# Optimization experiments

Hardware: AMD Instinct MI355X
Metric: run time of the kernel (lower is better)

The kernel has to match this reference:

```python
import jax, jax.numpy as jnp
import numpy as np

NUM_HEADS = 16


def setup_inputs() -> dict:
    key = jax.random.key(0)
    k1, k2, k3 = jax.random.split(key, 3)
    B, L, H = 2, 2048, 1024
    return {
        "key": jax.random.normal(k1, (B, L, H), dtype=jnp.float32),
        "W_ctx": jax.random.normal(k2, (H, H), dtype=jnp.float32) * (1.0 / np.sqrt(H)),
        "b_ctx": jax.random.normal(k3, (H,), dtype=jnp.float32) * 0.01,
    }


def reference(key, W_ctx, b_ctx):
    # Note: the torch module defines q/k/v Linear layers but never calls them
    # in forward(); it reshapes the raw input into heads directly.
    B, L, H = key.shape
    dh = H // NUM_HEADS
    # [B, L, H] -> [B, nh, L, dh]
    x = key.reshape(B, L, NUM_HEADS, dh).transpose(0, 2, 1, 3)
    # QK^T then scale by sqrt(head_dim) (key.shape[-1] after head split)
    scores = jnp.einsum("bhqd,bhkd->bhqk", x, x) * (1.0 / np.float32(np.sqrt(dh)))
    attn = jax.nn.softmax(scores, axis=-1)  # dropout p treated as eval/identity
    ctx = jnp.einsum("bhqk,bhkd->bhqd", attn, x)
    # [B, nh, L, dh] -> [B, L, H]
    ctx = ctx.transpose(0, 2, 1, 3).reshape(B, L, H)
    # context_transform: nn.Linear(H, H, bias=True)
    return ctx @ W_ctx.T + b_ctx
```

## Files before the change

kernel.cpp:

```cpp
#include <hip/hip_runtime.h>
#include <stdint.h>

#define NH     16
#define LSEQ   2048
#define DH     64
#define HDIM   1024
#define BATCH  2

typedef __attribute__((ext_vector_type(8))) short bf16x8;
typedef __attribute__((ext_vector_type(4))) short bf16x4;
typedef __attribute__((ext_vector_type(8))) unsigned short u16x8;
typedef __attribute__((ext_vector_type(4))) float f32x4;

static __device__ inline unsigned short f2bs(float f) {
    union { float f; uint32_t u; } v; v.f = f;
    uint32_t u = v.u;
    return (unsigned short)((u + 0x7FFFu + ((u >> 16) & 1u)) >> 16);
}
static __device__ inline float bf2f(unsigned short s) {
    return __uint_as_float(((uint32_t)s) << 16);
}

#define GLOAD_LDS(gp, lp) \
    __builtin_amdgcn_global_load_lds((const __attribute__((address_space(1))) void*)(gp), \
                                     (__attribute__((address_space(3))) void*)(lp), 16, 0, 0)

#define QK_SCALE 0.42466083f

__global__ __launch_bounds__(256) void cvt_kernel(const float* __restrict__ W,
                                                  unsigned short* __restrict__ Wb,
                                                  int n) {
    int i = (blockIdx.x * 256 + threadIdx.x) * 4;
    if (i < n) {
        float4 f = *(const float4*)(W + i);
        *(ushort4*)(Wb + i) = make_ushort4(f2bs(f.x), f2bs(f.y), f2bs(f.z), f2bs(f.w));
    }
}

__global__ __launch_bounds__(256) void xcvt_kernel(const float* __restrict__ x,
                                                   unsigned short* __restrict__ xb,
                                                   unsigned short* __restrict__ xt) {
    const int lt = blockIdx.x, bh = blockIdx.y;
    const int b = bh >> 4, h = bh & 15;
    const int t = threadIdx.x;
    const int r = t >> 2, cp = t & 3;

    __shared__ __align__(16) unsigned short Sm[64][72];

    const float* src = x + ((size_t)(b * LSEQ + lt * 64 + r)) * HDIM + h * DH + cp * 16;
    float4 f0 = *(const float4*)(src);
    float4 f1 = *(const float4*)(src + 4);
    float4 f2 = *(const float4*)(src + 8);
    float4 f3 = *(const float4*)(src + 12);
    u16x8 lo, hi;
    lo[0]=f2bs(f0.x); lo[1]=f2bs(f0.y); lo[2]=f2bs(f0.z); lo[3]=f2bs(f0.w);
    lo[4]=f2bs(f1.x); lo[5]=f2bs(f1.y); lo[6]=f2bs(f1.z); lo[7]=f2bs(f1.w);
    hi[0]=f2bs(f2.x); hi[1]=f2bs(f2.y); hi[2]=f2bs(f2.z); hi[3]=f2bs(f2.w);
    hi[4]=f2bs(f3.x); hi[5]=f2bs(f3.y); hi[6]=f2bs(f3.z); hi[7]=f2bs(f3.w);
    u16x8 slo, shi;
    slo[0]=f2bs(f0.x*QK_SCALE); slo[1]=f2bs(f0.y*QK_SCALE); slo[2]=f2bs(f0.z*QK_SCALE); slo[3]=f2bs(f0.w*QK_SCALE);
    slo[4]=f2bs(f1.x*QK_SCALE); slo[5]=f2bs(f1.y*QK_SCALE); slo[6]=f2bs(f1.z*QK_SCALE); slo[7]=f2bs(f1.w*QK_SCALE);
    shi[0]=f2bs(f2.x*QK_SCALE); shi[1]=f2bs(f2.y*QK_SCALE); shi[2]=f2bs(f2.z*QK_SCALE); shi[3]=f2bs(f2.w*QK_SCALE);
    shi[4]=f2bs(f3.x*QK_SCALE); shi[5]=f2bs(f3.y*QK_SCALE); shi[6]=f2bs(f3.z*QK_SCALE); shi[7]=f2bs(f3.w*QK_SCALE);

    {
        unsigned short* kt = xb + ((size_t)(bh * 32 + lt)) * 4096;
        const int s  = r >> 4, la = r & 15;
        const int ks = cp >> 1, q0 = (cp & 1) * 2;
        *(u16x8*)(kt + ((s * 2 + ks) * 64 + q0 * 16 + la) * 8)       = slo;
        *(u16x8*)(kt + ((s * 2 + ks) * 64 + (q0 + 1) * 16 + la) * 8) = shi;
    }
    *(u16x8*)&Sm[r][cp * 16]     = lo;
    *(u16x8*)&Sm[r][cp * 16 + 8] = hi;
    __syncthreads();

    {
        const int dt = t >> 6, lane = t & 63;
        const int la = lane & 15, quad = lane >> 4;
        u16x8 g0, g1;
        #pragma unroll
        for (int kvt = 0; kvt < 2; ++kvt)
            #pragma unroll
            for (int j = 0; j < 4; ++j)
                g0[kvt * 4 + j] = Sm[kvt * 16 + quad * 4 + j][dt * 16 + la];
        #pragma unroll
        for (int kvt = 0; kvt < 2; ++kvt)
            #pragma unroll
            for (int j = 0; j < 4; ++j)
                g1[kvt * 4 + j] = Sm[(kvt + 2) * 16 + quad * 4 + j][dt * 16 + la];
        unsigned short* vt = xt + ((size_t)(bh * 32 + lt)) * 4096;
        *(u16x8*)(vt + (dt * 64 + lane) * 16)     = g0;
        *(u16x8*)(vt + (dt * 64 + lane) * 16 + 8) = g1;
    }
}

__global__ __launch_bounds__(256) void attn_kernel(const unsigned short* __restrict__ xb,
                                                   const unsigned short* __restrict__ xt,
                                                   unsigned short* __restrict__ po,
                                                   float* __restrict__ pl) {
    const int bh = blockIdx.x;
    const int qt = blockIdx.y;
    const int ks = blockIdx.z;
    const int tid = threadIdx.x;
    const int w = tid >> 6, lane = tid & 63;
    const int la = lane & 15, quad = lane >> 4;

    __shared__ __align__(16) unsigned short KL[2][4096];
    __shared__ __align__(16) unsigned short VL[2][4096];

    const unsigned short* xbh = xb + (size_t)bh * 32 * 4096;
    const unsigned short* xth = xt + (size_t)bh * 32 * 4096;
    const int qbase = qt * 128 + w * 32;
    const int t0 = ks * 16;

    bf16x8 qf[2][2];
    #pragma unroll
    for (int qnt = 0; qnt < 2; ++qnt) {
        const int q0 = qbase + qnt * 16;
        const unsigned short* qs = xbh + (q0 >> 6) * 4096 + (((q0 >> 4) & 3) * 2) * 512;
        qf[qnt][0] = *(const bf16x8*)(qs + lane * 8);
        qf[qnt][1] = *(const bf16x8*)(qs + 512 + lane * 8);
    }

    const f32x4 fzero = {0.f, 0.f, 0.f, 0.f};
    f32x4 acc[2][4];
    #pragma unroll
    for (int i = 0; i < 2; ++i)
        #pragma unroll
        for (int j = 0; j < 4; ++j) acc[i][j] = fzero;
    float lp[2] = {0.f, 0.f};

    #pragma unroll
    for (int j = 0; j < 2; ++j) {
        const int off = (j * 256 + tid) * 16;
        GLOAD_LDS((const char*)(xbh + t0 * 4096) + off, (char*)KL[0] + off);
        GLOAD_LDS((const char*)(xth + t0 * 4096) + off, (char*)VL[0] + off);
    }
    __syncthreads();

    for (int tt = 0; tt < 16; ++tt) {
        if (tt < 15) {
            const char* ksrc = (const char*)(xbh + (t0 + tt + 1) * 4096);
            char* kdst = (char*)KL[(tt + 1) & 1];
            #pragma unroll
            for (int j = 0; j < 2; ++j) {
                const int off = (j * 256 + tid) * 16;
                GLOAD_LDS(ksrc + off, kdst + off);
            }
        }

        const unsigned short* kb = KL[tt & 1];
        f32x4 st[4][2];
        #pragma unroll
        for (int kvt = 0; kvt < 4; ++kvt) {
            bf16x8 kf0 = *(const bf16x8*)(kb + (kvt * 2 + 0) * 512 + lane * 8);
            bf16x8 kf1 = *(const bf16x8*)(kb + (kvt * 2 + 1) * 512 + lane * 8);
            #pragma unroll
            for (int qnt = 0; qnt < 2; ++qnt) {
                f32x4 s = fzero;
                s = __builtin_amdgcn_mfma_f32_16x16x32_bf16(kf0, qf[qnt][0], s, 0, 0, 0);
                s = __builtin_amdgcn_mfma_f32_16x16x32_bf16(kf1, qf[qnt][1], s, 0, 0, 0);
                st[kvt][qnt] = s;
            }
        }

        bf16x4 pf[2][4];
        #pragma unroll
        for (int qnt = 0; qnt < 2; ++qnt) {
            float ls = 0.f;
            #pragma unroll
            for (int kvt = 0; kvt < 4; ++kvt) {
                float p0 = __builtin_amdgcn_exp2f(st[kvt][qnt][0]);
                float p1 = __builtin_amdgcn_exp2f(st[kvt][qnt][1]);
                float p2 = __builtin_amdgcn_exp2f(st[kvt][qnt][2]);
                float p3 = __builtin_amdgcn_exp2f(st[kvt][qnt][3]);
                ls += (p0 + p1) + (p2 + p3);
                uint32_t u0 = __float_as_uint(p0) + 0x8000u;
                uint32_t u1 = __float_as_uint(p1) + 0x8000u;
                uint32_t u2 = __float_as_uint(p2) + 0x8000u;
                uint32_t u3 = __float_as_uint(p3) + 0x8000u;
                union { uint2 u; bf16x4 v; } cv;
                cv.u = make_uint2(__builtin_amdgcn_perm(u1, u0, 0x07060302),
                                  __builtin_amdgcn_perm(u3, u2, 0x07060302));
                pf[qnt][kvt] = cv.v;
            }
            lp[qnt] += ls;
        }

        __syncthreads();

        if (tt < 15) {
            const char* vsrc = (const char*)(xth + (t0 + tt + 1) * 4096);
            char* vdst = (char*)VL[(tt + 1) & 1];
            #pragma unroll
            for (int j = 0; j < 2; ++j) {
                const int off = (j * 256 + tid) * 16;
                GLOAD_LDS(vsrc + off, vdst + off);
            }
        }

        const unsigned short* vb = VL[tt & 1];
        #pragma unroll
        for (int dt = 0; dt < 4; ++dt) {
            const unsigned short* vrow = vb + (dt * 64 + lane) * 16;
            #pragma unroll
            for (int kvt = 0; kvt < 4; ++kvt) {
                bf16x4 vf = *(const bf16x4*)(vrow + kvt * 4);
                #pragma unroll
                for (int qnt = 0; qnt < 2; ++qnt)
                    acc[qnt][dt] = __builtin_amdgcn_mfma_f32_16x16x16bf16_1k(
                        vf, pf[qnt][kvt], acc[qnt][dt], 0, 0, 0);
            }
        }
    }

    const size_t prow = (size_t)(ks * 32 + bh) * 2048 + qbase;
    unsigned short* pob = po + prow * 64;
    #pragma unroll
    for (int qnt = 0; qnt < 2; ++qnt) {
        unsigned short* orow = pob + (size_t)(qnt * 16 + la) * 64 + quad * 4;
        #pragma unroll
        for (int dt = 0; dt < 4; ++dt) {
            f32x4 a = acc[qnt][dt];
            *(ushort4*)(orow + dt * 16) =
                make_ushort4(f2bs(a[0]), f2bs(a[1]), f2bs(a[2]), f2bs(a[3]));
        }
    }
    #pragma unroll
    for (int qnt = 0; qnt < 2; ++qnt) {
        float l = lp[qnt];
        l += __shfl_xor(l, 16);
        l += __shfl_xor(l, 32);
        if (quad == 0) pl[prow + qnt * 16 + la] = l;
    }
}

__global__ __launch_bounds__(256) void reduce_kernel(const unsigned short* __restrict__ po,
                                                     const float* __restrict__ pl,
                                                     unsigned short* __restrict__ ctx) {
    const int gid = blockIdx.x * 256 + threadIdx.x;
    const int rid = gid >> 4;
    const int d0  = (gid & 15) * 4;
    const float invl = 1.0f / (pl[rid] + pl[65536 + rid]);
    ushort4 a = *(const ushort4*)(po + (size_t)rid * 64 + d0);
    ushort4 c = *(const ushort4*)(po + (size_t)65536 * 64 + (size_t)rid * 64 + d0);
    const int bh = rid >> 11, q = rid & 2047;
    const int b = bh >> 4, h = bh & 15;
    unsigned short* dst = ctx + (((size_t)(b * 2048 + q) * 16 + h) * 64) + d0;
    *(ushort4*)dst = make_ushort4(
        f2bs((bf2f(a.x) + bf2f(c.x)) * invl),
        f2bs((bf2f(a.y) + bf2f(c.y)) * invl),
        f2bs((bf2f(a.z) + bf2f(c.z)) * invl),
        f2bs((bf2f(a.w) + bf2f(c.w)) * invl));
}

__global__ __launch_bounds__(256) void proj_kernel(const unsigned short* __restrict__ A,
                                                   const unsigned short* __restrict__ Bw,
                                                   const float* __restrict__ bias,
                                                   float* __restrict__ out) {
    const int n0 = blockIdx.x * 64;
    const int m0 = blockIdx.y * 128;
    const int tid = threadIdx.x;
    const int w = tid >> 6, lane = tid & 63;
    const int la = lane & 15, quad = lane >> 4;
    const int wm = (w >> 1) * 64, wn = (w & 1) * 32;
    const int K = HDIM;

    __shared__ __align__(16) unsigned short As[128 * 32];
    __shared__ __align__(16) unsigned short Bs[64 * 32];

    const f32x4 fzero = {0.f, 0.f, 0.f, 0.f};
    f32x4 acc[4][2];
    #pragma unroll
    for (int i = 0; i < 4; ++i)
        #pragma unroll
        for (int j = 0; j < 2; ++j) acc[i][j] = fzero;

    for (int k0 = 0; k0 < K; k0 += 32) {
        __syncthreads();
        #pragma unroll
        for (int j = 0; j < 2; ++j) {
            const int fc = j * 256 + tid;
            GLOAD_LDS(A + (size_t)(m0 + (fc >> 2)) * K + k0 + (fc & 3) * 8, (char*)As + fc * 16);
        }
        GLOAD_LDS(Bw + (size_t)(n0 + (tid >> 2)) * K + k0 + (tid & 3) * 8, (char*)Bs + tid * 16);
        __syncthreads();

        bf16x8 af[4], bfr[2];
        #pragma unroll
        for (int mt = 0; mt < 4; ++mt) af[mt]  = *(const bf16x8*)&As[(wm + mt * 16 + la) * 32 + quad * 8];
        #pragma unroll
        for (int nt = 0; nt < 2; ++nt) bfr[nt] = *(const bf16x8*)&Bs[(wn + nt * 16 + la) * 32 + quad * 8];
        #pragma unroll
        for (int mt = 0; mt < 4; ++mt)
            #pragma unroll
            for (int nt = 0; nt < 2; ++nt)
                acc[mt][nt] = __builtin_amdgcn_mfma_f32_16x16x32_bf16(af[mt], bfr[nt], acc[mt][nt], 0, 0, 0);
    }

    #pragma unroll
    for (int nt = 0; nt < 2; ++nt) {
        const int n = n0 + wn + nt * 16 + la;
        const float bv = bias[n];
        #pragma unroll
        for (int mt = 0; mt < 4; ++mt)
            #pragma unroll
            for (int r = 0; r < 4; ++r) {
                const int m = m0 + wm + mt * 16 + quad * 4 + r;
                out[(size_t)m * HDIM + n] = acc[mt][nt][r] + bv;
            }
    }
}

extern "C" void kernel_launch(void* const* d_in, const int* in_sizes, int n_in,
                              void* d_out, int out_size, void* d_ws, size_t ws_size,
                              hipStream_t stream) {
    const float* x    = (const float*)d_in[0];
    const float* W    = (const float*)d_in[1];
    const float* bias = (const float*)d_in[2];
    float* out = (float*)d_out;

    unsigned short* ctx = (unsigned short*)d_ws;
    unsigned short* xbp = (unsigned short*)((char*)d_ws + ( 8u << 20));
    unsigned short* xtp = (unsigned short*)((char*)d_ws + (16u << 20));
    unsigned short* Wb  = (unsigned short*)((char*)d_ws + (24u << 20));
    unsigned short* po  = (unsigned short*)((char*)d_ws + (26u << 20));
    float*          pl  = (float*)         ((char*)d_ws + (42u << 20));

    cvt_kernel<<<dim3(HDIM * HDIM / 1024), 256, 0, stream>>>(W, Wb, HDIM * HDIM);
    xcvt_kernel<<<dim3(32, 32), 256, 0, stream>>>(x, xbp, xtp);
    attn_kernel<<<dim3(32, 16, 2), 256, 0, stream>>>(xbp, xtp, po, pl);
    reduce_kernel<<<dim3(4096), 256, 0, stream>>>(po, pl, ctx);
    proj_kernel<<<dim3(16, 32), 256, 0, stream>>>(ctx, Wb, bias, out);
}
```

Baseline: 157.4 us.

## Pre-tile and swizzle GEMM operands, enlarge proj tiles, make KV split configurable

The weight conversion and reduce kernels now write bf16 operands in a pre-tiled, XOR-swizzled 128x64 block layout. This lets the projection GEMM load contiguous tiles with double-buffered global-to-LDS copies, 128x128 output tiles and BK=64, which should cut LDS bank conflicts and per-iteration barriers. The attention KV split becomes runtime-configurable (4 splits if the workspace is large enough, else 2) to raise the number of attention blocks, at the cost of more partial outputs to reduce. The larger proj tiles halve the grid to 256 blocks, which may underfill the GPU.

```diff
diff --git a/kernel.cpp b/kernel.cpp
--- a/kernel.cpp
+++ b/kernel.cpp
@@ -28,13 +28,19 @@
 #define QK_SCALE 0.42466083f
 
 __global__ __launch_bounds__(256) void cvt_kernel(const float* __restrict__ W,
-                                                  unsigned short* __restrict__ Wb,
-                                                  int n) {
-    int i = (blockIdx.x * 256 + threadIdx.x) * 4;
-    if (i < n) {
-        float4 f = *(const float4*)(W + i);
-        *(ushort4*)(Wb + i) = make_ushort4(f2bs(f.x), f2bs(f.y), f2bs(f.z), f2bs(f.w));
-    }
+                                                  unsigned short* __restrict__ wbt) {
+    const int gid = blockIdx.x * 256 + threadIdx.x;
+    const int n  = gid >> 7;
+    const int kc = gid & 127;
+    const float* src = W + (size_t)n * 1024 + kc * 8;
+    float4 f0 = *(const float4*)(src);
+    float4 f1 = *(const float4*)(src + 4);
+    u16x8 v;
+    v[0]=f2bs(f0.x); v[1]=f2bs(f0.y); v[2]=f2bs(f0.z); v[3]=f2bs(f0.w);
+    v[4]=f2bs(f1.x); v[5]=f2bs(f1.y); v[6]=f2bs(f1.z); v[7]=f2bs(f1.w);
+    const int nt = n >> 7, rn = n & 127;
+    const int kt = kc >> 3, c = kc & 7;
+    *(u16x8*)(wbt + (((size_t)nt * 16 + kt) * 128 + rn) * 64 + ((c ^ (rn & 7)) * 8)) = v;
 }
 
 __global__ __launch_bounds__(256) void xcvt_kernel(const float* __restrict__ x,
@@ -97,10 +103,11 @@
 __global__ __launch_bounds__(256) void attn_kernel(const unsigned short* __restrict__ xb,
                                                    const unsigned short* __restrict__ xt,
                                                    unsigned short* __restrict__ po,
-                                                   float* __restrict__ pl) {
+                                                   float* __restrict__ pl,
+                                                   int nt_tiles) {
     const int bh = blockIdx.x;
     const int qt = blockIdx.y;
-    const int ks = blockIdx.z;
+    const int ksb = blockIdx.z;
     const int tid = threadIdx.x;
     const int w = tid >> 6, lane = tid & 63;
     const int la = lane & 15, quad = lane >> 4;
@@ -111,7 +118,7 @@
     const unsigned short* xbh = xb + (size_t)bh * 32 * 4096;
     const unsigned short* xth = xt + (size_t)bh * 32 * 4096;
     const int qbase = qt * 128 + w * 32;
-    const int t0 = ks * 16;
+    const int t0 = ksb * nt_tiles;
 
     bf16x8 qf[2][2];
     #pragma unroll
@@ -138,8 +145,8 @@
     }
     __syncthreads();
 
-    for (int tt = 0; tt < 16; ++tt) {
-        if (tt < 15) {
+    for (int tt = 0; tt < nt_tiles; ++tt) {
+        if (tt < nt_tiles - 1) {
             const char* ksrc = (const char*)(xbh + (t0 + tt + 1) * 4096);
             char* kdst = (char*)KL[(tt + 1) & 1];
             #pragma unroll
@@ -189,7 +196,7 @@
 
         __syncthreads();
 
-        if (tt < 15) {
+        if (tt < nt_tiles - 1) {
             const char* vsrc = (const char*)(xth + (t0 + tt + 1) * 4096);
             char* vdst = (char*)VL[(tt + 1) & 1];
             #pragma unroll
@@ -214,7 +221,7 @@
         }
     }
 
-    const size_t prow = (size_t)(ks * 32 + bh) * 2048 + qbase;
+    const size_t prow = (size_t)(ksb * 32 + bh) * 2048 + qbase;
     unsigned short* pob = po + prow * 64;
     #pragma unroll
     for (int qnt = 0; qnt < 2; ++qnt) {
@@ -237,69 +244,100 @@
 
 __global__ __launch_bounds__(256) void reduce_kernel(const unsigned short* __restrict__ po,
                                                      const float* __restrict__ pl,
-                                                     unsigned short* __restrict__ ctx) {
+                                                     unsigned short* __restrict__ ctxt,
+                                                     int KS) {
     const int gid = blockIdx.x * 256 + threadIdx.x;
     const int rid = gid >> 4;
     const int d0  = (gid & 15) * 4;
-    const float invl = 1.0f / (pl[rid] + pl[65536 + rid]);
-    ushort4 a = *(const ushort4*)(po + (size_t)rid * 64 + d0);
-    ushort4 c = *(const ushort4*)(po + (size_t)65536 * 64 + (size_t)rid * 64 + d0);
+    float l = 0.f;
+    for (int s = 0; s < KS; ++s) l += pl[(size_t)s * 65536 + rid];
+    const float invl = 1.0f / l;
+    float o0 = 0.f, o1 = 0.f, o2 = 0.f, o3 = 0.f;
+    for (int s = 0; s < KS; ++s) {
+        ushort4 a = *(const ushort4*)(po + ((size_t)s * 65536 + rid) * 64 + d0);
+        o0 += bf2f(a.x); o1 += bf2f(a.y); o2 += bf2f(a.z); o3 += bf2f(a.w);
+    }
     const int bh = rid >> 11, q = rid & 2047;
     const int b = bh >> 4, h = bh & 15;
-    unsigned short* dst = ctx + (((size_t)(b * 2048 + q) * 16 + h) * 64) + d0;
-    *(ushort4*)dst = make_ushort4(
-        f2bs((bf2f(a.x) + bf2f(c.x)) * invl),
-        f2bs((bf2f(a.y) + bf2f(c.y)) * invl),
-        f2bs((bf2f(a.z) + bf2f(c.z)) * invl),
-        f2bs((bf2f(a.w) + bf2f(c.w)) * invl));
-}
-
-__global__ __launch_bounds__(256) void proj_kernel(const unsigned short* __restrict__ A,
-                                                   const unsigned short* __restrict__ Bw,
+    const int m = b * 2048 + q;
+    const int mt = m >> 7, r = m & 127;
+    const int c = d0 >> 3, off = d0 & 7;
+    unsigned short* dst = ctxt + (((size_t)mt * 16 + h) * 128 + r) * 64 + ((c ^ (r & 7)) * 8) + off;
+    *(ushort4*)dst = make_ushort4(f2bs(o0 * invl), f2bs(o1 * invl),
+                                  f2bs(o2 * invl), f2bs(o3 * invl));
+}
+
+__global__ __launch_bounds__(256) void proj_kernel(const unsigned short* __restrict__ ctxt,
+                                                   const unsigned short* __restrict__ wbt,
                                                    const float* __restrict__ bias,
                                                    float* __restrict__ out) {
-    const int n0 = blockIdx.x * 64;
-    const int m0 = blockIdx.y * 128;
+    const int ntb = blockIdx.x;
+    const int mtb = blockIdx.y;
     const int tid = threadIdx.x;
     const int w = tid >> 6, lane = tid & 63;
     const int la = lane & 15, quad = lane >> 4;
-    const int wm = (w >> 1) * 64, wn = (w & 1) * 32;
-    const int K = HDIM;
-
-    __shared__ __align__(16) unsigned short As[128 * 32];
-    __shared__ __align__(16) unsigned short Bs[64 * 32];
+    const int wm = (w >> 1) * 64, wn = (w & 1) * 64;
+
+    __shared__ __align__(16) unsigned short As[2][8192];
+    __shared__ __align__(16) unsigned short Bs[2][8192];
+
+    const unsigned short* abase = ctxt + (size_t)mtb * 16 * 8192;
+    const unsigned short* bbase = wbt  + (size_t)ntb * 16 * 8192;
+
+    const int sw0 = ((quad)     ^ (la & 7)) * 8;
+    const int sw1 = ((quad + 4) ^ (la & 7)) * 8;
 
     const f32x4 fzero = {0.f, 0.f, 0.f, 0.f};
-    f32x4 acc[4][2];
+    f32x4 acc[4][4];
     #pragma unroll
     for (int i = 0; i < 4; ++i)
         #pragma unroll
-        for (int j = 0; j < 2; ++j) acc[i][j] = fzero;
-
-    for (int k0 = 0; k0 < K; k0 += 32) {
+        for (int j = 0; j < 4; ++j) acc[i][j] = fzero;
+
+    #pragma unroll
+    for (int j = 0; j < 4; ++j) {
+        const int fc = j * 256 + tid;
+        GLOAD_LDS((const char*)abase + fc * 16, (char*)As[0] + fc * 16);
+        GLOAD_LDS((const char*)bbase + fc * 16, (char*)Bs[0] + fc * 16);
+    }
+    __syncthreads();
+
+    for (int kt = 0; kt < 16; ++kt) {
+        if (kt < 15) {
+            const char* asrc = (const char*)(abase + (kt + 1) * 8192);
+            const char* bsrc = (const char*)(bbase + (kt + 1) * 8192);
+            char* adst = (char*)As[(kt + 1) & 1];
+            char* bdst = (char*)Bs[(kt + 1) & 1];
+            #pragma unroll
+            for (int j = 0; j < 4; ++j) {
+                const int fc = j * 256 + tid;
+                GLOAD_LDS(asrc + fc * 16, adst + fc * 16);
+                GLOAD_LDS(bsrc + fc * 16, bdst + fc * 16);
+            }
+        }
+
+        const unsigned short* Ab = As[kt & 1];
+        const unsigned short* Bb = Bs[kt & 1];
+        #pragma unroll
+        for (int ks2 = 0; ks2 < 2; ++ks2) {
+            const int sw = ks2 ? sw1 : sw0;
+            bf16x8 af[4], bfr[4];
+            #pragma unroll
+            for (int mt = 0; mt < 4; ++mt) af[mt]  = *(const bf16x8*)&Ab[(wm + mt * 16 + la) * 64 + sw];
+            #pragma unroll
+            for (int nt = 0; nt < 4; ++nt) bfr[nt] = *(const bf16x8*)&Bb[(wn + nt * 16 + la) * 64 + sw];
+            #pragma unroll
+            for (int mt = 0; mt < 4; ++mt)
+                #pragma unroll
+                for (int nt = 0; nt < 4; ++nt)
+                    acc[mt][nt] = __builtin_amdgcn_mfma_f32_16x16x32_bf16(af[mt], bfr[nt], acc[mt][nt], 0, 0, 0);
+        }
         __syncthreads();
-        #pragma unroll
-        for (int j = 0; j < 2; ++j) {
-            const int fc = j * 256 + tid;
-            GLOAD_LDS(A + (size_t)(m0 + (fc >> 2)) * K + k0 + (fc & 3) * 8, (char*)As + fc * 16);
-        }
-        GLOAD_LDS(Bw + (size_t)(n0 + (tid >> 2)) * K + k0 + (tid & 3) * 8, (char*)Bs + tid * 16);
-        __syncthreads();
-
-        bf16x8 af[4], bfr[2];
-        #pragma unroll
-        for (int mt = 0; mt < 4; ++mt) af[mt]  = *(const bf16x8*)&As[(wm + mt * 16 + la) * 32 + quad * 8];
-        #pragma unroll
-        for (int nt = 0; nt < 2; ++nt) bfr[nt] = *(const bf16x8*)&Bs[(wn + nt * 16 + la) * 32 + quad * 8];
-        #pragma unroll
-        for (int mt = 0; mt < 4; ++mt)
-            #pragma unroll
-            for (int nt = 0; nt < 2; ++nt)
-                acc[mt][nt] = __builtin_amdgcn_mfma_f32_16x16x32_bf16(af[mt], bfr[nt], acc[mt][nt], 0, 0, 0);
-    }
-
-    #pragma unroll
-    for (int nt = 0; nt < 2; ++nt) {
+    }
+
+    const int m0 = mtb * 128, n0 = ntb * 128;
+    #pragma unroll
+    for (int nt = 0; nt < 4; ++nt) {
         const int n = n0 + wn + nt * 16 + la;
         const float bv = bias[n];
         #pragma unroll
@@ -320,16 +358,18 @@
     const float* bias = (const float*)d_in[2];
     float* out = (float*)d_out;
 
-    unsigned short* ctx = (unsigned short*)d_ws;
-    unsigned short* xbp = (unsigned short*)((char*)d_ws + ( 8u << 20));
-    unsigned short* xtp = (unsigned short*)((char*)d_ws + (16u << 20));
-    unsigned short* Wb  = (unsigned short*)((char*)d_ws + (24u << 20));
-    unsigned short* po  = (unsigned short*)((char*)d_ws + (26u << 20));
-    float*          pl  = (float*)         ((char*)d_ws + (42u << 20));
-
-    cvt_kernel<<<dim3(HDIM * HDIM / 1024), 256, 0, stream>>>(W, Wb, HDIM * HDIM);
+    const int KS = (ws_size >= (60u << 20)) ? 4 : 2;
+
+    unsigned short* ctxt = (unsigned short*)d_ws;
+    unsigned short* xbp  = (unsigned short*)((char*)d_ws + ( 8u << 20));
+    unsigned short* xtp  = (unsigned short*)((char*)d_ws + (16u << 20));
+    unsigned short* wbt  = (unsigned short*)((char*)d_ws + (24u << 20));
+    float*          pl   = (float*)         ((char*)d_ws + (26u << 20));
+    unsigned short* po   = (unsigned short*)((char*)d_ws + (27u << 20));
+
+    cvt_kernel<<<dim3(512), 256, 0, stream>>>(W, wbt);
     xcvt_kernel<<<dim3(32, 32), 256, 0, stream>>>(x, xbp, xtp);
-    attn_kernel<<<dim3(32, 16, 2), 256, 0, stream>>>(xbp, xtp, po, pl);
-    reduce_kernel<<<dim3(4096), 256, 0, stream>>>(po, pl, ctx);
-    proj_kernel<<<dim3(16, 32), 256, 0, stream>>>(ctx, Wb, bias, out);
-}
+    attn_kernel<<<dim3(32, 16, KS), 256, 0, stream>>>(xbp, xtp, po, pl, 32 / KS);
+    reduce_kernel<<<dim3(4096), 256, 0, stream>>>(po, pl, ctxt, KS);
+    proj_kernel<<<dim3(8, 32), 256, 0, stream>>>(ctxt, wbt, bias, out);
+}
```

Result: no change. 159.4 us (+1.3%).
